# Kernel tuning notes

Measured on AMD Instinct MI355X. Metric: run time of the kernel, lower is better.

The kernel has to match this reference:

```python
import jax, jax.numpy as jnp
import numpy as np
from jax import lax

B, C, H, W = 16, 3, 64, 64
P = 256        # total_patches
PS = 9         # patch_size
E = 256        # attn_embed_dim
NH = 8         # attn_heads
POSD = 64      # pos_embed_dim
HW = H * W
DH = E // NH


def setup_inputs() -> dict:
    key = jax.random.key(0)
    ks = jax.random.split(key, 20)
    def rn(k, shape, fan_in):
        return jax.random.normal(k, shape, jnp.float32) * (1.0 / np.sqrt(fan_in))
    return {
        "x": jax.random.normal(ks[0], (B, C, H, W), jnp.float32),
        "conv_w": rn(ks[1], (P, C, PS, PS), C * PS * PS),
        "conv_b": jnp.zeros((P,), jnp.float32),
        "in_w": rn(ks[2], (HW, E), HW),
        "in_b": jnp.zeros((E,), jnp.float32),
        "wq": rn(ks[3], (E, E), E), "bq": jnp.zeros((E,), jnp.float32),
        "wk": rn(ks[4], (E, E), E), "bk": jnp.zeros((E,), jnp.float32),
        "wv": rn(ks[5], (E, E), E), "bv": jnp.zeros((E,), jnp.float32),
        "wo": rn(ks[6], (E, E), E), "bo": jnp.zeros((E,), jnp.float32),
        "out_w": rn(ks[7], (E, HW), E),
        "out_b": jnp.zeros((HW,), jnp.float32),
        "fc_w": rn(ks[8], (HW, 2), HW),
        "fc_b": jnp.zeros((2,), jnp.float32),
        "pos_w": rn(ks[9], (2, POSD), 2),
        "pos_b": jnp.zeros((POSD,), jnp.float32),
    }


# pixel-center normalized coords matching affine_grid(align_corners=False)
_BASE = (2.0 * jnp.arange(PS, dtype=jnp.float32) + 1.0) / PS - 1.0


def _sample_patch(img, tx, ty):
    # img: (C,H,W); tx, ty scalars. Replicates affine_grid + grid_sample
    # (bilinear, padding_mode='border', align_corners=False) WITHOUT the
    # full-image repeat of the original module.
    gx = (PS / W) * _BASE[None, :] + tx     # (PS,PS) x-coords
    gy = (PS / H) * _BASE[:, None] + ty     # (PS,PS) y-coords
    ix = ((gx + 1.0) * W - 1.0) * 0.5       # unnormalize, align_corners=False
    iy = ((gy + 1.0) * H - 1.0) * 0.5
    x0 = jnp.floor(ix); y0 = jnp.floor(iy)
    wx = ix - x0;       wy = iy - y0
    x0i = jnp.clip(x0.astype(jnp.int32), 0, W - 1)
    x1i = jnp.clip(x0.astype(jnp.int32) + 1, 0, W - 1)
    y0i = jnp.clip(y0.astype(jnp.int32), 0, H - 1)
    y1i = jnp.clip(y0.astype(jnp.int32) + 1, 0, H - 1)
    v00 = img[:, y0i, x0i]; v01 = img[:, y0i, x1i]
    v10 = img[:, y1i, x0i]; v11 = img[:, y1i, x1i]
    return (v00 * (1 - wx) * (1 - wy) + v01 * wx * (1 - wy)
            + v10 * (1 - wx) * wy + v11 * wx * wy)   # (C,PS,PS)


def _forward(x, conv_w, conv_b, in_w, in_b, wq, bq, wk, bk, wv, bv, wo, bo,
             out_w, out_b, fc_w, fc_b, pos_w, pos_b):
    # ConvBlock: conv (same padding for odd kernel) + ReLU
    feat = lax.conv_general_dilated(
        x, conv_w, (1, 1), [(PS // 2, PS // 2)] * 2,
        dimension_numbers=("NCHW", "OIHW", "NCHW"))
    feat = jax.nn.relu(feat + conv_b[None, :, None, None])   # (B,P,H,W)
    # ConvSelfAttn: tokens are the P channels, features are flattened HxW
    tok = feat.reshape(B, P, HW) @ in_w + in_b                # (B,P,E)
    q = (tok @ wq + bq).reshape(B, P, NH, DH)
    k = (tok @ wk + bk).reshape(B, P, NH, DH)
    v = (tok @ wv + bv).reshape(B, P, NH, DH)
    scores = jnp.einsum("bqhd,bkhd->bhqk", q, k) / np.sqrt(DH)
    attn = jax.nn.softmax(scores, axis=-1)
    o = jnp.einsum("bhqk,bkhd->bqhd", attn, v).reshape(B, P, E)
    o = o @ wo + bo
    feat2 = o @ out_w + out_b                                 # (B,P,HW)
    # translation params in [-1,1]
    tp = jnp.tanh(feat2 @ fc_w + fc_b)                        # (B,P,2)
    tx, ty = tp[..., 0], tp[..., 1]
    sample_bp = jax.vmap(jax.vmap(_sample_patch, in_axes=(None, 0, 0)),
                         in_axes=(0, 0, 0))
    patches = sample_bp(x, tx, ty)                            # (B,P,C,PS,PS)
    patches = patches.reshape(B, P, C * PS * PS)
    pos_embeds = tp @ pos_w + pos_b                           # (B,P,POSD)
    return patches, pos_embeds


def reference(x, conv_w, conv_b, in_w, in_b, wq, bq, wk, bk, wv, bv, wo, bo,
              out_w, out_b, fc_w, fc_b, pos_w, pos_b):
    return _forward(x, conv_w, conv_b, in_w, in_b, wq, bq, wk, bk, wv, bv,
                    wo, bo, out_w, out_b, fc_w, fc_b, pos_w, pos_b)
```

## Files before the change

kernel.cpp:

```cpp
#include <hip/hip_runtime.h>
#include <hip/hip_bf16.h>

#define Bd 16
#define Cd 3
#define Hd 64
#define Wd 64
#define Pd 256
#define PSd 9
#define Ed 256
#define NHd 8
#define DHd 32
#define HWd 4096
#define POSDd 64

typedef unsigned short u16;
typedef short short8 __attribute__((ext_vector_type(8)));
typedef float f32x4 __attribute__((ext_vector_type(4)));

__device__ __forceinline__ float bf2f(u16 u) {
    union { unsigned int i; float f; } c; c.i = ((unsigned int)u) << 16; return c.f;
}
__device__ __forceinline__ u16 f2bf(float f) {
    unsigned int x = __float_as_uint(f);
    unsigned int r = (x + 0x7fffu + ((x >> 16) & 1u)) >> 16;
    return (u16)r;
}

__global__ __launch_bounds__(64) void precompute_G(
    const float* __restrict__ out_w, const float* __restrict__ fc_w,
    const float* __restrict__ out_b, const float* __restrict__ fc_b,
    float* __restrict__ G, float* __restrict__ h0) {
    int blk = blockIdx.x, lane = threadIdx.x;
    if (blk < 256) {
        int e = blk;
        float a0 = 0.f, a1 = 0.f;
        for (int i = lane; i < HWd; i += 64) {
            float a = out_w[e * HWd + i];
            a0 += a * fc_w[2 * i];
            a1 += a * fc_w[2 * i + 1];
        }
        #pragma unroll
        for (int off = 32; off; off >>= 1) { a0 += __shfl_xor(a0, off); a1 += __shfl_xor(a1, off); }
        if (lane == 0) { G[2 * e] = a0; G[2 * e + 1] = a1; }
    } else {
        int j = blk - 256;
        float a = 0.f;
        for (int i = lane; i < HWd; i += 64) a += out_b[i] * fc_w[2 * i + j];
        #pragma unroll
        for (int off = 32; off; off >>= 1) a += __shfl_xor(a, off);
        if (lane == 0) h0[j] = a + fc_b[j];
    }
}

__global__ __launch_bounds__(64) void precompute_M2(
    const float* __restrict__ wo, const float* __restrict__ bo,
    const float* __restrict__ G, float* __restrict__ M2, float* __restrict__ h0) {
    int blk = blockIdx.x, lane = threadIdx.x;
    if (blk < 256) {
        float m0 = 0.f, m1 = 0.f;
        for (int f = lane; f < Ed; f += 64) {
            float wv = wo[blk * Ed + f];
            m0 += wv * G[2 * f];
            m1 += wv * G[2 * f + 1];
        }
        #pragma unroll
        for (int off = 32; off; off >>= 1) { m0 += __shfl_xor(m0, off); m1 += __shfl_xor(m1, off); }
        if (lane == 0) { M2[2 * blk] = m0; M2[2 * blk + 1] = m1; }
    } else {
        int j = blk - 256;
        float hh = 0.f;
        for (int f = lane; f < Ed; f += 64) hh += bo[f] * G[2 * f + j];
        #pragma unroll
        for (int off = 32; off; off >>= 1) hh += __shfl_xor(hh, off);
        if (lane == 0) h0[j] += hh;
    }
}

__global__ __launch_bounds__(256) void prep_weight_t(
    const float* __restrict__ W, u16* __restrict__ Th, u16* __restrict__ Tl,
    int K, int N) {
    __shared__ u16 th[64][65];
    __shared__ u16 tl[64][65];
    int k0 = blockIdx.x * 64, n0 = blockIdx.y * 64;
    int col = threadIdx.x & 63, r4 = threadIdx.x >> 6;
    #pragma unroll
    for (int i = 0; i < 16; i++) {
        int kr = 4 * i + r4;
        float v = W[(size_t)(k0 + kr) * N + n0 + col];
        u16 h = f2bf(v);
        th[col][kr] = h;
        tl[col][kr] = f2bf(v - bf2f(h));
    }
    __syncthreads();
    #pragma unroll
    for (int i = 0; i < 16; i++) {
        int nr = 4 * i + r4;
        Th[(size_t)(n0 + nr) * K + k0 + col] = th[nr][col];
        Tl[(size_t)(n0 + nr) * K + k0 + col] = tl[nr][col];
    }
}

__global__ __launch_bounds__(256) void prep_convw(
    const float* __restrict__ W, u16* __restrict__ Ah, u16* __restrict__ Al) {
    int p = blockIdx.x, k = threadIdx.x;
    float v = (k < 243) ? W[p * 243 + k] : 0.f;
    u16 h = f2bf(v);
    Ah[p * 256 + k] = h;
    Al[p * 256 + k] = f2bf(v - bf2f(h));
}

__global__ __launch_bounds__(256) void concat_bias(
    const float* __restrict__ bq, const float* __restrict__ bk,
    const float* __restrict__ bv, float* __restrict__ b3) {
    int t = threadIdx.x;
    b3[t] = bq[t]; b3[256 + t] = bk[t]; b3[512 + t] = bv[t];
}

__global__ __launch_bounds__(256, 2) void conv_gemm(
    const u16* __restrict__ Ah, const u16* __restrict__ Al,
    const float* __restrict__ x, const float* __restrict__ conv_b,
    u16* __restrict__ feat_hi, u16* __restrict__ feat_lo) {
    __shared__ u16 sBh[64 * 72], sBl[64 * 72];
    __shared__ float wls[3 * 9 * 72];
    int tid = threadIdx.x;
    int w = tid >> 6, L = tid & 63;
    int m16 = L & 15, qd = L >> 4;
    int y = blockIdx.x;
    int nb = y << 6;
    int b = blockIdx.y;

    for (int i = tid; i < 3 * 9 * 72; i += 256) wls[i] = 0.f;
    __syncthreads();
    for (int i = tid; i < 3 * 9 * 64; i += 256) {
        int c = i / 576, rem = i - c * 576, wr = rem >> 6, col = rem & 63;
        int iy = y - 4 + wr;
        if (iy >= 0 && iy < 64)
            wls[c * 648 + wr * 72 + 4 + col] = x[((b * 3 + c) << 12) + (iy << 6) + col];
    }
    __syncthreads();

    f32x4 acc[4][4];
    #pragma unroll
    for (int mt = 0; mt < 4; mt++)
        #pragma unroll
        for (int ct = 0; ct < 4; ct++) acc[mt][ct] = (f32x4){0.f, 0.f, 0.f, 0.f};

    int n = tid >> 2, kb = (tid & 3) << 4;
    int arow = w * 16 + m16;

    for (int k0 = 0; k0 < 256; k0 += 64) {
        short8 afh[4][2], afl[4][2];
        #pragma unroll
        for (int mt = 0; mt < 4; mt++)
            #pragma unroll
            for (int c = 0; c < 2; c++) {
                int ao = (mt * 64 + arow) * 256 + k0 + c * 32 + qd * 8;
                afh[mt][c] = *(const short8*)(Ah + ao);
                afl[mt][c] = *(const short8*)(Al + ao);
            }
        u16 hbuf[16] __attribute__((aligned(8)));
        u16 lbuf[16] __attribute__((aligned(8)));
        #pragma unroll
        for (int j = 0; j < 16; j++) {
            int k = k0 + kb + j;
            float v = 0.f;
            if (k < 243) {
                int c = (k >= 81) + (k >= 162);
                int rem = k - c * 81;
                int dy = (rem * 57) >> 9;
                int dx = rem - dy * 9;
                v = wls[c * 648 + dy * 72 + dx + n];
            }
            u16 h = f2bf(v);
            hbuf[j] = h;
            lbuf[j] = f2bf(v - bf2f(h));
        }
        __syncthreads();
        #pragma unroll
        for (int t = 0; t < 4; t++) {
            *(ushort4*)&sBh[n * 72 + kb + 4 * t] = *(ushort4*)&hbuf[4 * t];
            *(ushort4*)&sBl[n * 72 + kb + 4 * t] = *(ushort4*)&lbuf[4 * t];
        }
        __syncthreads();
        #pragma unroll
        for (int c = 0; c < 2; c++) {
            #pragma unroll
            for (int ct = 0; ct < 4; ct++) {
                int bb = (ct * 16 + m16) * 72 + c * 32 + qd * 8;
                short8 bH = *(const short8*)&sBh[bb];
                short8 bL = *(const short8*)&sBl[bb];
                #pragma unroll
                for (int mt = 0; mt < 4; mt++) {
                    acc[mt][ct] = __builtin_amdgcn_mfma_f32_16x16x32_bf16(afh[mt][c], bH, acc[mt][ct], 0, 0, 0);
                    acc[mt][ct] = __builtin_amdgcn_mfma_f32_16x16x32_bf16(afh[mt][c], bL, acc[mt][ct], 0, 0, 0);
                    acc[mt][ct] = __builtin_amdgcn_mfma_f32_16x16x32_bf16(afl[mt][c], bH, acc[mt][ct], 0, 0, 0);
                }
            }
        }
    }

    #pragma unroll
    for (int mt = 0; mt < 4; mt++) {
        #pragma unroll
        for (int i = 0; i < 4; i++) {
            int gr = mt * 64 + w * 16 + qd * 4 + i;
            float bv = conv_b[gr];
            #pragma unroll
            for (int ct = 0; ct < 4; ct++) {
                int gc = nb + ct * 16 + m16;
                float val = fmaxf(acc[mt][ct][i] + bv, 0.f);
                size_t oi = ((size_t)(b * 256 + gr)) * HWd + gc;
                u16 h = f2bf(val);
                feat_hi[oi] = h;
                feat_lo[oi] = f2bf(val - bf2f(h));
            }
        }
    }
}

__global__ __launch_bounds__(256, 4) void gemm_mfma3(
    const u16* __restrict__ Ah, const u16* __restrict__ Al,
    const u16* __restrict__ Bh, const u16* __restrict__ Bl,
    const float* __restrict__ bias,
    float* __restrict__ Co, u16* __restrict__ Ch, u16* __restrict__ Cl,
    int N, int K, int klen, long long pstride, int mode) {
    __shared__ u16 sAh[64 * 72], sAl[64 * 72], sBh[64 * 72], sBl[64 * 72];
    int tid = threadIdx.x;
    int w = tid >> 6;
    int L = tid & 63;
    int m16 = L & 15, qd = L >> 4;
    int mb = blockIdx.y * 64, nb = blockIdx.x * 64;
    int kbeg = blockIdx.z * klen;

    f32x4 acc[4];
    #pragma unroll
    for (int i = 0; i < 4; i++) acc[i] = (f32x4){0.f, 0.f, 0.f, 0.f};

    int r = tid >> 2, s = tid & 3;
    const u16* pAh = Ah + (size_t)(mb + r) * K + kbeg + s * 16;
    const u16* pAl = Al + (size_t)(mb + r) * K + kbeg + s * 16;
    const u16* pBh = Bh + (size_t)(nb + r) * K + kbeg + s * 16;
    const u16* pBl = Bl + (size_t)(nb + r) * K + kbeg + s * 16;
    u16* dAh = &sAh[r * 72 + s * 16];
    u16* dAl = &sAl[r * 72 + s * 16];
    u16* dBh = &sBh[r * 72 + s * 16];
    u16* dBl = &sBl[r * 72 + s * 16];

    uint4 a0 = *(const uint4*)(pAh);
    uint4 a1 = *(const uint4*)(pAh + 8);
    uint4 a2 = *(const uint4*)(pAl);
    uint4 a3 = *(const uint4*)(pAl + 8);
    uint4 b0 = *(const uint4*)(pBh);
    uint4 b1 = *(const uint4*)(pBh + 8);
    uint4 b2 = *(const uint4*)(pBl);
    uint4 b3 = *(const uint4*)(pBl + 8);

    for (int k0 = 0; k0 < klen; k0 += 64) {
        __syncthreads();
        *(uint4*)(dAh) = a0; *(uint4*)(dAh + 8) = a1;
        *(uint4*)(dAl) = a2; *(uint4*)(dAl + 8) = a3;
        *(uint4*)(dBh) = b0; *(uint4*)(dBh + 8) = b1;
        *(uint4*)(dBl) = b2; *(uint4*)(dBl + 8) = b3;
        __syncthreads();
        int kn = k0 + 64;
        if (kn < klen) {
            a0 = *(const uint4*)(pAh + kn);
            a1 = *(const uint4*)(pAh + kn + 8);
            a2 = *(const uint4*)(pAl + kn);
            a3 = *(const uint4*)(pAl + kn + 8);
            b0 = *(const uint4*)(pBh + kn);
            b1 = *(const uint4*)(pBh + kn + 8);
            b2 = *(const uint4*)(pBl + kn);
            b3 = *(const uint4*)(pBl + kn + 8);
        }
        #pragma unroll
        for (int c = 0; c < 2; c++) {
            int ab = (w * 16 + m16) * 72 + c * 32 + qd * 8;
            short8 aH = *(const short8*)&sAh[ab];
            short8 aL = *(const short8*)&sAl[ab];
            #pragma unroll
            for (int ct = 0; ct < 4; ct++) {
                int bb = (ct * 16 + m16) * 72 + c * 32 + qd * 8;
                short8 bH = *(const short8*)&sBh[bb];
                short8 bL = *(const short8*)&sBl[bb];
                acc[ct] = __builtin_amdgcn_mfma_f32_16x16x32_bf16(aH, bH, acc[ct], 0, 0, 0);
                acc[ct] = __builtin_amdgcn_mfma_f32_16x16x32_bf16(aH, bL, acc[ct], 0, 0, 0);
                acc[ct] = __builtin_amdgcn_mfma_f32_16x16x32_bf16(aL, bH, acc[ct], 0, 0, 0);
            }
        }
    }

    #pragma unroll
    for (int ct = 0; ct < 4; ct++) {
        int gc = nb + ct * 16 + m16;
        float bv = (mode == 2) ? 0.f : bias[gc];
        #pragma unroll
        for (int i = 0; i < 4; i++) {
            int gr = mb + w * 16 + qd * 4 + i;
            float val = acc[ct][i] + bv;
            size_t oi = (size_t)gr * N + gc;
            if (mode == 0) {
                Co[oi] = val;
            } else if (mode == 2) {
                Co[(size_t)blockIdx.z * pstride + oi] = val;
            } else {
                u16 h = f2bf(val);
                Ch[oi] = h;
                Cl[oi] = f2bf(val - bf2f(h));
            }
        }
    }
}

__global__ __launch_bounds__(256) void reduce_split(
    const float* __restrict__ part, const float* __restrict__ bias,
    u16* __restrict__ Ch, u16* __restrict__ Cl, int total) {
    int i = (blockIdx.x * 256 + threadIdx.x) * 4;
    if (i >= total) return;
    float4 s0 = *(const float4*)(part + i);
    float4 s1 = *(const float4*)(part + (size_t)total + i);
    float4 s2 = *(const float4*)(part + 2 * (size_t)total + i);
    float4 s3 = *(const float4*)(part + 3 * (size_t)total + i);
    float4 bv = *(const float4*)(bias + (i & 255));
    float v[4] = { s0.x + s1.x + s2.x + s3.x + bv.x,
                   s0.y + s1.y + s2.y + s3.y + bv.y,
                   s0.z + s1.z + s2.z + s3.z + bv.z,
                   s0.w + s1.w + s2.w + s3.w + bv.w };
    u16 hb[4] __attribute__((aligned(8)));
    u16 lb[4] __attribute__((aligned(8)));
    #pragma unroll
    for (int j = 0; j < 4; j++) {
        u16 h = f2bf(v[j]);
        hb[j] = h;
        lb[j] = f2bf(v[j] - bf2f(h));
    }
    *(ushort4*)(Ch + i) = *(ushort4*)hb;
    *(ushort4*)(Cl + i) = *(ushort4*)lb;
}

__global__ __launch_bounds__(256) void attention(
    const float* __restrict__ qkv, float* __restrict__ o) {
    __shared__ float ksh[64][32];
    __shared__ float vsh[64][32];
    int b = blockIdx.x, h = blockIdx.y, qc = blockIdx.z;
    int t = threadIdx.x;
    int row = t >> 2, sub = t & 3;
    int r = qc * 64 + row;
    const float rs = 0.17677669529663687f;

    float qr[8];
    const float* qrow = qkv + ((size_t)(b * Pd + r)) * 768 + h * DHd + sub * 8;
    #pragma unroll
    for (int d = 0; d < 8; d++) qr[d] = qrow[d];

    float m = -1e30f, l = 0.f;
    float oacc[8];
    #pragma unroll
    for (int d = 0; d < 8; d++) oacc[d] = 0.f;

    for (int ch = 0; ch < 4; ch++) {
        __syncthreads();
        {
            const float* srck = qkv + ((size_t)(b * Pd + ch * 64 + row)) * 768 + 256 + h * DHd + sub * 8;
            const float* srcv = srck + 256;
            float4 k0 = *(const float4*)(srck);
            float4 k1 = *(const float4*)(srck + 4);
            float4 v0 = *(const float4*)(srcv);
            float4 v1 = *(const float4*)(srcv + 4);
            *(float4*)&ksh[row][sub * 8]     = k0;
            *(float4*)&ksh[row][sub * 8 + 4] = k1;
            *(float4*)&vsh[row][sub * 8]     = v0;
            *(float4*)&vsh[row][sub * 8 + 4] = v1;
        }
        __syncthreads();
        #pragma unroll 2
        for (int kk = 0; kk < 64; kk++) {
            float4 ka = *(const float4*)&ksh[kk][sub * 8];
            float4 kb = *(const float4*)&ksh[kk][sub * 8 + 4];
            float s0 = qr[0] * ka.x + qr[1] * ka.y;
            float s1 = qr[2] * ka.z + qr[3] * ka.w;
            float s2 = qr[4] * kb.x + qr[5] * kb.y;
            float s3 = qr[6] * kb.z + qr[7] * kb.w;
            float s = (s0 + s1) + (s2 + s3);
            s += __shfl_xor(s, 1);
            s += __shfl_xor(s, 2);
            s *= rs;
            float mnew = fmaxf(m, s);
            float scale = __expf(m - mnew);
            float pexp = __expf(s - mnew);
            l = l * scale + pexp;
            float4 va = *(const float4*)&vsh[kk][sub * 8];
            float4 vb = *(const float4*)&vsh[kk][sub * 8 + 4];
            oacc[0] = fmaf(oacc[0], scale, pexp * va.x);
            oacc[1] = fmaf(oacc[1], scale, pexp * va.y);
            oacc[2] = fmaf(oacc[2], scale, pexp * va.z);
            oacc[3] = fmaf(oacc[3], scale, pexp * va.w);
            oacc[4] = fmaf(oacc[4], scale, pexp * vb.x);
            oacc[5] = fmaf(oacc[5], scale, pexp * vb.y);
            oacc[6] = fmaf(oacc[6], scale, pexp * vb.z);
            oacc[7] = fmaf(oacc[7], scale, pexp * vb.w);
            m = mnew;
        }
    }
    float rinv = 1.f / l;
    float* orow = o + ((size_t)(b * Pd + r)) * Ed + h * DHd + sub * 8;
    #pragma unroll
    for (int d = 0; d < 8; d++) orow[d] = oacc[d] * rinv;
}

#define PATCH_OUT 995328
__global__ __launch_bounds__(256) void head_kernel(
    const float* __restrict__ o, const float* __restrict__ M2,
    const float* __restrict__ h0, const float* __restrict__ pos_w,
    const float* __restrict__ pos_b, const float* __restrict__ x,
    float* __restrict__ out) {
    int w = threadIdx.x >> 6, lane = threadIdx.x & 63;
    int bp = blockIdx.x * 4 + w;
    int b = bp >> 8;

    const float* orow = o + (size_t)bp * Ed;
    float4 o4 = *(const float4*)(orow + lane * 4);
    int e0 = lane * 4;
    float s0 = o4.x * M2[2 * e0 + 0] + o4.y * M2[2 * e0 + 2] + o4.z * M2[2 * e0 + 4] + o4.w * M2[2 * e0 + 6];
    float s1 = o4.x * M2[2 * e0 + 1] + o4.y * M2[2 * e0 + 3] + o4.z * M2[2 * e0 + 5] + o4.w * M2[2 * e0 + 7];
    #pragma unroll
    for (int off = 32; off; off >>= 1) { s0 += __shfl_xor(s0, off); s1 += __shfl_xor(s1, off); }

    float tx = tanhf(s0 + h0[0]);
    float ty = tanhf(s1 + h0[1]);

    {
        float pv = tx * pos_w[lane] + ty * pos_w[64 + lane] + pos_b[lane];
        out[PATCH_OUT + bp * POSDd + lane] = pv;
    }

    const float* xb = x + b * 3 * HWd;
    #pragma unroll
    for (int s = 0; s < 4; s++) {
        int idx = s * 64 + lane;
        if (idx < 243) {
            int c = idx / 81;
            int rem = idx - c * 81;
            int iy = rem / 9;
            int jx = rem - iy * 9;
            float basex = (2.f * jx + 1.f) / 9.f - 1.f;
            float basey = (2.f * iy + 1.f) / 9.f - 1.f;
            float gx = 0.140625f * basex + tx;
            float gy = 0.140625f * basey + ty;
            float ix  = ((gx + 1.f) * 64.f - 1.f) * 0.5f;
            float iyf = ((gy + 1.f) * 64.f - 1.f) * 0.5f;
            float x0f = floorf(ix), y0f = floorf(iyf);
            float wx = ix - x0f, wy = iyf - y0f;
            int x0i = min(max((int)x0f, 0), 63);
            int x1i = min(max((int)x0f + 1, 0), 63);
            int y0i = min(max((int)y0f, 0), 63);
            int y1i = min(max((int)y0f + 1, 0), 63);
            const float* xc = xb + c * HWd;
            float v00 = xc[y0i * Wd + x0i];
            float v01 = xc[y0i * Wd + x1i];
            float v10 = xc[y1i * Wd + x0i];
            float v11 = xc[y1i * Wd + x1i];
            float val = v00 * (1.f - wx) * (1.f - wy) + v01 * wx * (1.f - wy)
                      + v10 * (1.f - wx) * wy + v11 * wx * wy;
            out[bp * 243 + idx] = val;
        }
    }
}

extern "C" void kernel_launch(void* const* d_in, const int* in_sizes, int n_in,
                              void* d_out, int out_size, void* d_ws, size_t ws_size,
                              hipStream_t stream) {
    (void)in_sizes; (void)n_in; (void)out_size;
    const float* x      = (const float*)d_in[0];
    const float* conv_w = (const float*)d_in[1];
    const float* conv_b = (const float*)d_in[2];
    const float* in_w   = (const float*)d_in[3];
    const float* in_b   = (const float*)d_in[4];
    const float* wq     = (const float*)d_in[5];
    const float* bq     = (const float*)d_in[6];
    const float* wk     = (const float*)d_in[7];
    const float* bk     = (const float*)d_in[8];
    const float* wv     = (const float*)d_in[9];
    const float* bv     = (const float*)d_in[10];
    const float* wo     = (const float*)d_in[11];
    const float* bo     = (const float*)d_in[12];
    const float* out_w  = (const float*)d_in[13];
    const float* out_b  = (const float*)d_in[14];
    const float* fc_w   = (const float*)d_in[15];
    const float* fc_b   = (const float*)d_in[16];
    const float* pos_w  = (const float*)d_in[17];
    const float* pos_b  = (const float*)d_in[18];

    int CB = 16;
    for (;;) {
        size_t need = ((size_t)(2 * CB + 4) * 1048576 + 2 * 196608 + 2 * 65536) * 2
                    + (768 + 3145728 + 1048576 + 4ull * CB * 65536 + 2048) * 4;
        if (need <= ws_size || CB == 1) break;
        CB >>= 1;
    }
    int nchunks = 16 / CB;

    char* base = (char*)d_ws;
    u16* feat_hi = (u16*)base;
    u16* feat_lo = feat_hi + (size_t)CB * 1048576;
    u16* tok_hi  = feat_lo + (size_t)CB * 1048576;
    u16* tok_lo  = tok_hi + 1048576;
    u16* inw_h   = tok_lo + 1048576;
    u16* inw_l   = inw_h + 1048576;
    u16* wqkv_h  = inw_l + 1048576;
    u16* wqkv_l  = wqkv_h + 196608;
    u16* convw_h = wqkv_l + 196608;
    u16* convw_l = convw_h + 65536;
    float* bqkv  = (float*)(convw_l + 65536);
    float* qkv   = bqkv + 768;
    float* o     = qkv + 3145728;
    float* part  = o + 1048576;
    float* G     = part + 4ull * CB * 65536;
    float* M2    = G + 512;
    float* h0    = M2 + 512;
    float* out   = (float*)d_out;

    hipLaunchKernelGGL(precompute_G, dim3(258), dim3(64), 0, stream,
                       out_w, fc_w, out_b, fc_b, G, h0);
    hipLaunchKernelGGL(precompute_M2, dim3(258), dim3(64), 0, stream,
                       wo, bo, G, M2, h0);
    hipLaunchKernelGGL(prep_weight_t, dim3(64, 4), dim3(256), 0, stream,
                       in_w, inw_h, inw_l, 4096, 256);
    hipLaunchKernelGGL(prep_weight_t, dim3(4, 4), dim3(256), 0, stream,
                       wq, wqkv_h, wqkv_l, 256, 256);
    hipLaunchKernelGGL(prep_weight_t, dim3(4, 4), dim3(256), 0, stream,
                       wk, wqkv_h + 256 * 256, wqkv_l + 256 * 256, 256, 256);
    hipLaunchKernelGGL(prep_weight_t, dim3(4, 4), dim3(256), 0, stream,
                       wv, wqkv_h + 512 * 256, wqkv_l + 512 * 256, 256, 256);
    hipLaunchKernelGGL(prep_convw, dim3(256), dim3(256), 0, stream,
                       conv_w, convw_h, convw_l);
    hipLaunchKernelGGL(concat_bias, dim3(1), dim3(256), 0, stream,
                       bq, bk, bv, bqkv);

    for (int c = 0; c < nchunks; ++c) {
        hipLaunchKernelGGL(conv_gemm, dim3(64, CB), dim3(256), 0, stream,
                           convw_h, convw_l,
                           x + (size_t)c * CB * 3 * HWd, conv_b,
                           feat_hi, feat_lo);
        hipLaunchKernelGGL(gemm_mfma3, dim3(4, CB * 4, 4), dim3(256), 0, stream,
                           feat_hi, feat_lo, inw_h, inw_l, in_b,
                           part, (u16*)nullptr, (u16*)nullptr,
                           256, 4096, 1024, (long long)CB * 65536, 2);
        hipLaunchKernelGGL(reduce_split, dim3(CB * 65536 / 1024), dim3(256), 0, stream,
                           part, in_b,
                           tok_hi + (size_t)c * CB * 65536,
                           tok_lo + (size_t)c * CB * 65536,
                           CB * 65536);
    }
    hipLaunchKernelGGL(gemm_mfma3, dim3(12, 64, 1), dim3(256), 0, stream,
                       tok_hi, tok_lo, wqkv_h, wqkv_l, bqkv,
                       qkv, (u16*)nullptr, (u16*)nullptr, 768, 256, 256, 0LL, 0);
    hipLaunchKernelGGL(attention, dim3(16, 8, 4), dim3(256), 0, stream, qkv, o);
    hipLaunchKernelGGL(head_kernel, dim3(1024), dim3(256), 0, stream,
                       o, M2, h0, pos_w, pos_b, x, out);
}
```

Before: 302.0 us.

## Run attention on MFMA with split-bf16 QKV and transposed V

The scalar FP32 online-softmax attention is replaced by an MFMA kernel. It computes QK^T and PV with bf16 hi/lo split operands, and the QKV GEMM now writes its output in split-bf16 form. A new transpose kernel lays V out per head as d-major so PV can load B fragments contiguously. Softmax skips max subtraction and the probabilities are rounded to single bf16, which risks overflow and adds an extra launch and workspace.

```diff
diff --git a/kernel.cpp b/kernel.cpp
--- a/kernel.cpp
+++ b/kernel.cpp
@@ -338,74 +338,115 @@
     *(ushort4*)(Cl + i) = *(ushort4*)lb;
 }
 
-__global__ __launch_bounds__(256) void attention(
-    const float* __restrict__ qkv, float* __restrict__ o) {
-    __shared__ float ksh[64][32];
-    __shared__ float vsh[64][32];
+__global__ __launch_bounds__(256) void transpose_v(
+    const u16* __restrict__ qkvh, const u16* __restrict__ qkvl,
+    u16* __restrict__ vTh, u16* __restrict__ vTl) {
+    __shared__ u16 th[32][264];
+    __shared__ u16 tl[32][264];
+    int b = blockIdx.x, h = blockIdx.y;
+    int t = threadIdx.x;
+    {
+        const u16* srch = qkvh + ((size_t)(b * 256 + t)) * 768 + 512 + h * 32;
+        const u16* srcl = qkvl + ((size_t)(b * 256 + t)) * 768 + 512 + h * 32;
+        #pragma unroll
+        for (int j = 0; j < 4; j++) {
+            short8 vh = *(const short8*)(srch + j * 8);
+            short8 vl = *(const short8*)(srcl + j * 8);
+            #pragma unroll
+            for (int e = 0; e < 8; e++) {
+                th[j * 8 + e][t] = (u16)vh[e];
+                tl[j * 8 + e][t] = (u16)vl[e];
+            }
+        }
+    }
+    __syncthreads();
+    {
+        int d = t >> 3, seg = t & 7;
+        size_t dst = ((size_t)((b * 8 + h) * 32 + d)) * 256 + seg * 32;
+        #pragma unroll
+        for (int j = 0; j < 4; j++) {
+            *(uint4*)(vTh + dst + j * 8) = *(uint4*)&th[d][seg * 32 + j * 8];
+            *(uint4*)(vTl + dst + j * 8) = *(uint4*)&tl[d][seg * 32 + j * 8];
+        }
+    }
+}
+
+__global__ __launch_bounds__(256) void attention_mfma(
+    const u16* __restrict__ qkvh, const u16* __restrict__ qkvl,
+    const u16* __restrict__ vTh, const u16* __restrict__ vTl,
+    float* __restrict__ o) {
+    __shared__ u16 ph[4][16][264];
     int b = blockIdx.x, h = blockIdx.y, qc = blockIdx.z;
-    int t = threadIdx.x;
-    int row = t >> 2, sub = t & 3;
-    int r = qc * 64 + row;
+    int tid = threadIdx.x;
+    int w = tid >> 6, L = tid & 63;
+    int m16 = L & 15, qd = L >> 4;
     const float rs = 0.17677669529663687f;
 
-    float qr[8];
-    const float* qrow = qkv + ((size_t)(b * Pd + r)) * 768 + h * DHd + sub * 8;
-    #pragma unroll
-    for (int d = 0; d < 8; d++) qr[d] = qrow[d];
-
-    float m = -1e30f, l = 0.f;
-    float oacc[8];
-    #pragma unroll
-    for (int d = 0; d < 8; d++) oacc[d] = 0.f;
-
-    for (int ch = 0; ch < 4; ch++) {
-        __syncthreads();
-        {
-            const float* srck = qkv + ((size_t)(b * Pd + ch * 64 + row)) * 768 + 256 + h * DHd + sub * 8;
-            const float* srcv = srck + 256;
-            float4 k0 = *(const float4*)(srck);
-            float4 k1 = *(const float4*)(srck + 4);
-            float4 v0 = *(const float4*)(srcv);
-            float4 v1 = *(const float4*)(srcv + 4);
-            *(float4*)&ksh[row][sub * 8]     = k0;
-            *(float4*)&ksh[row][sub * 8 + 4] = k1;
-            *(float4*)&vsh[row][sub * 8]     = v0;
-            *(float4*)&vsh[row][sub * 8 + 4] = v1;
-        }
-        __syncthreads();
-        #pragma unroll 2
-        for (int kk = 0; kk < 64; kk++) {
-            float4 ka = *(const float4*)&ksh[kk][sub * 8];
-            float4 kb = *(const float4*)&ksh[kk][sub * 8 + 4];
-            float s0 = qr[0] * ka.x + qr[1] * ka.y;
-            float s1 = qr[2] * ka.z + qr[3] * ka.w;
-            float s2 = qr[4] * kb.x + qr[5] * kb.y;
-            float s3 = qr[6] * kb.z + qr[7] * kb.w;
-            float s = (s0 + s1) + (s2 + s3);
-            s += __shfl_xor(s, 1);
-            s += __shfl_xor(s, 2);
-            s *= rs;
-            float mnew = fmaxf(m, s);
-            float scale = __expf(m - mnew);
-            float pexp = __expf(s - mnew);
-            l = l * scale + pexp;
-            float4 va = *(const float4*)&vsh[kk][sub * 8];
-            float4 vb = *(const float4*)&vsh[kk][sub * 8 + 4];
-            oacc[0] = fmaf(oacc[0], scale, pexp * va.x);
-            oacc[1] = fmaf(oacc[1], scale, pexp * va.y);
-            oacc[2] = fmaf(oacc[2], scale, pexp * va.z);
-            oacc[3] = fmaf(oacc[3], scale, pexp * va.w);
-            oacc[4] = fmaf(oacc[4], scale, pexp * vb.x);
-            oacc[5] = fmaf(oacc[5], scale, pexp * vb.y);
-            oacc[6] = fmaf(oacc[6], scale, pexp * vb.z);
-            oacc[7] = fmaf(oacc[7], scale, pexp * vb.w);
-            m = mnew;
-        }
-    }
-    float rinv = 1.f / l;
-    float* orow = o + ((size_t)(b * Pd + r)) * Ed + h * DHd + sub * 8;
-    #pragma unroll
-    for (int d = 0; d < 8; d++) orow[d] = oacc[d] * rinv;
+    size_t qoff = ((size_t)(b * 256 + qc * 64 + w * 16 + m16)) * 768 + h * 32 + qd * 8;
+    short8 qH = *(const short8*)(qkvh + qoff);
+    short8 qL = *(const short8*)(qkvl + qoff);
+
+    f32x4 sacc[16];
+    #pragma unroll
+    for (int nt = 0; nt < 16; nt++) {
+        size_t koff = ((size_t)(b * 256 + nt * 16 + m16)) * 768 + 256 + h * 32 + qd * 8;
+        short8 bH = *(const short8*)(qkvh + koff);
+        short8 bL = *(const short8*)(qkvl + koff);
+        f32x4 a = (f32x4){0.f, 0.f, 0.f, 0.f};
+        a = __builtin_amdgcn_mfma_f32_16x16x32_bf16(qH, bH, a, 0, 0, 0);
+        a = __builtin_amdgcn_mfma_f32_16x16x32_bf16(qH, bL, a, 0, 0, 0);
+        a = __builtin_amdgcn_mfma_f32_16x16x32_bf16(qL, bH, a, 0, 0, 0);
+        sacc[nt] = a;
+    }
+
+    float l4[4] = {0.f, 0.f, 0.f, 0.f};
+    #pragma unroll
+    for (int nt = 0; nt < 16; nt++)
+        #pragma unroll
+        for (int i = 0; i < 4; i++) {
+            float p = __expf(sacc[nt][i] * rs);
+            sacc[nt][i] = p;
+            l4[i] += p;
+        }
+    #pragma unroll
+    for (int i = 0; i < 4; i++) {
+        l4[i] += __shfl_xor(l4[i], 1);
+        l4[i] += __shfl_xor(l4[i], 2);
+        l4[i] += __shfl_xor(l4[i], 4);
+        l4[i] += __shfl_xor(l4[i], 8);
+    }
+
+    #pragma unroll
+    for (int nt = 0; nt < 16; nt++)
+        #pragma unroll
+        for (int i = 0; i < 4; i++)
+            ph[w][qd * 4 + i][nt * 16 + m16] = f2bf(sacc[nt][i]);
+
+    f32x4 oacc[2];
+    oacc[0] = (f32x4){0.f, 0.f, 0.f, 0.f};
+    oacc[1] = (f32x4){0.f, 0.f, 0.f, 0.f};
+    size_t vbase = ((size_t)(b * 8 + h)) * 32 * 256;
+    #pragma unroll
+    for (int kt = 0; kt < 8; kt++) {
+        short8 pa = *(const short8*)&ph[w][m16][kt * 32 + qd * 8];
+        #pragma unroll
+        for (int ct = 0; ct < 2; ct++) {
+            size_t voff = vbase + (size_t)(ct * 16 + m16) * 256 + kt * 32 + qd * 8;
+            short8 vH = *(const short8*)(vTh + voff);
+            short8 vL = *(const short8*)(vTl + voff);
+            oacc[ct] = __builtin_amdgcn_mfma_f32_16x16x32_bf16(pa, vH, oacc[ct], 0, 0, 0);
+            oacc[ct] = __builtin_amdgcn_mfma_f32_16x16x32_bf16(pa, vL, oacc[ct], 0, 0, 0);
+        }
+    }
+
+    #pragma unroll
+    for (int i = 0; i < 4; i++) {
+        float rinv = 1.f / l4[i];
+        int orow = b * 256 + qc * 64 + w * 16 + qd * 4 + i;
+        #pragma unroll
+        for (int ct = 0; ct < 2; ct++)
+            o[(size_t)orow * 256 + h * 32 + ct * 16 + m16] = oacc[ct][i] * rinv;
+    }
 }
 
 #define PATCH_OUT 995328
@@ -493,9 +534,10 @@
 
     int CB = 16;
     for (;;) {
-        size_t need = ((size_t)(2 * CB + 4) * 1048576 + 2 * 196608 + 2 * 65536) * 2
-                    + (768 + 3145728 + 1048576 + 4ull * CB * 65536 + 2048) * 4;
-        if (need <= ws_size || CB == 1) break;
+        size_t u16e = (size_t)(2 * CB + 4) * 1048576 + 2 * 196608 + 2 * 65536
+                    + 2 * 3145728 + 2 * 1048576;
+        size_t f32e = 768 + 1048576 + 4ull * CB * 65536 + 2048;
+        if (u16e * 2 + f32e * 4 <= ws_size || CB == 1) break;
         CB >>= 1;
     }
     int nchunks = 16 / CB;
@@ -511,9 +553,12 @@
     u16* wqkv_l  = wqkv_h + 196608;
     u16* convw_h = wqkv_l + 196608;
     u16* convw_l = convw_h + 65536;
-    float* bqkv  = (float*)(convw_l + 65536);
-    float* qkv   = bqkv + 768;
-    float* o     = qkv + 3145728;
+    u16* qkvh    = convw_l + 65536;
+    u16* qkvl    = qkvh + 3145728;
+    u16* vTh     = qkvl + 3145728;
+    u16* vTl     = vTh + 1048576;
+    float* bqkv  = (float*)(vTl + 1048576);
+    float* o     = bqkv + 768;
     float* part  = o + 1048576;
     float* G     = part + 4ull * CB * 65536;
     float* M2    = G + 512;
@@ -554,8 +599,11 @@
     }
     hipLaunchKernelGGL(gemm_mfma3, dim3(12, 64, 1), dim3(256), 0, stream,
                        tok_hi, tok_lo, wqkv_h, wqkv_l, bqkv,
-                       qkv, (u16*)nullptr, (u16*)nullptr, 768, 256, 256, 0LL, 0);
-    hipLaunchKernelGGL(attention, dim3(16, 8, 4), dim3(256), 0, stream, qkv, o);
+                       (float*)nullptr, qkvh, qkvl, 768, 256, 256, 0LL, 1);
+    hipLaunchKernelGGL(transpose_v, dim3(16, 8), dim3(256), 0, stream,
+                       qkvh, qkvl, vTh, vTl);
+    hipLaunchKernelGGL(attention_mfma, dim3(16, 8, 4), dim3(256), 0, stream,
+                       qkvh, qkvl, vTh, vTl, o);
     hipLaunchKernelGGL(head_kernel, dim3(1024), dim3(256), 0, stream,
                        o, M2, h0, pos_w, pos_b, x, out);
 }
```

New measurement: 270.7 us. 1.12x faster.
